# Kernel tuning notes

Measured on AMD Instinct MI355X. Metric: run time of the kernel, lower is better.

## Reference

```python
import jax, jax.numpy as jnp
import numpy as np
import math

NUM_HEADS = 16
FOCUS_FACTOR = 1.35  # 1.0 + congestion_level(0.3) + packet_loss(0.05)


def setup_inputs() -> dict:
    key = jax.random.key(0)
    ks = jax.random.split(key, 6)
    B, S, D = 2, 2048, 1024
    s = 1.0 / math.sqrt(D)
    return {
        "x": jax.random.normal(ks[0], (B, S, D), jnp.float32),
        "mask": jnp.ones((B, 1, S, S), jnp.int32),
        "Wq": jax.random.normal(ks[1], (D, D), jnp.float32) * s,
        "bq": jnp.zeros((D,), jnp.float32),
        "Wk": jax.random.normal(ks[2], (D, D), jnp.float32) * s,
        "bk": jnp.zeros((D,), jnp.float32),
        "Wv": jax.random.normal(ks[3], (D, D), jnp.float32) * s,
        "bv": jnp.zeros((D,), jnp.float32),
        "Wo": jax.random.normal(ks[4], (D, D), jnp.float32) * s,
        "bo": jnp.zeros((D,), jnp.float32),
    }


def reference(x, mask, Wq, bq, Wk, bk, Wv, bv, Wo, bo):
    B, S, D = x.shape
    H = NUM_HEADS
    hd = D // H
    # linear projections (torch Linear: x @ W^T + b), split heads -> [B,H,S,hd]
    q = (x @ Wq.T + bq).reshape(B, S, H, hd).transpose(0, 2, 1, 3)
    k = (x @ Wk.T + bk).reshape(B, S, H, hd).transpose(0, 2, 1, 3)
    v = (x @ Wv.T + bv).reshape(B, S, H, hd).transpose(0, 2, 1, 3)
    # rotary embedding in the source is an identity pass-through
    scores = jnp.einsum("bhqd,bhkd->bhqk", q, k) / math.sqrt(hd)
    scores = jnp.where(mask == 0, jnp.float32(-1e9), scores)
    scores = scores * jnp.float32(FOCUS_FACTOR)  # network focus factor
    attn = jax.nn.softmax(scores, axis=-1)  # dropout is identity in eval
    attended = jnp.einsum("bhqk,bhkd->bhqd", attn, v)
    attended = attended.transpose(0, 2, 1, 3).reshape(B, S, D)
    out = attended @ Wo.T + bo
    avg_attention = attn.mean(axis=1)  # [B, S, S]
    return out, avg_attention
```

## Files before the change

### kernel.cpp

```cpp
#include <hip/hip_runtime.h>
#include <cstdint>

typedef __bf16 bf16x8 __attribute__((ext_vector_type(8)));
typedef __bf16 bf16x4 __attribute__((ext_vector_type(4)));
typedef short  s16x8  __attribute__((ext_vector_type(8)));
typedef float  f32x4  __attribute__((ext_vector_type(4)));
typedef unsigned int uint32;
typedef uint32 u32x2 __attribute__((ext_vector_type(2)));
typedef unsigned long long u64;

#define SB 2048
#define DD 1024
#define HH 16
#define HDD 64
#define BB 2
#define C2LOG 0.2434547882f
#define NEGBIG2 (-1.9476383e9f)

__device__ __forceinline__ ushort f2bf(float f){
  uint32 u = __builtin_bit_cast(uint32, f);
  u += 0x7fffu + ((u >> 16) & 1u);
  return (ushort)(u >> 16);
}
__device__ __forceinline__ bf16x8 ldb128(const void* p){
  return __builtin_bit_cast(bf16x8, *(const s16x8*)p);
}
__device__ __forceinline__ void gl_lds16(const void* g, void* l){
  __builtin_amdgcn_global_load_lds((const __attribute__((address_space(1))) void*)g,
                                   (__attribute__((address_space(3))) void*)l, 16, 0, 0);
}
__device__ __forceinline__ float exp2r(float x){
  float r; asm("v_exp_f32 %0, %1" : "=v"(r) : "v"(x)); return r;
}

__global__ __launch_bounds__(256) void k_prep(
    const float* __restrict__ x, const int* __restrict__ mask,
    const float* __restrict__ Wq, const float* __restrict__ Wk,
    const float* __restrict__ Wv, const float* __restrict__ Wo,
    ushort* __restrict__ xb, u64* __restrict__ bits,
    ushort* __restrict__ wqb, ushort* __restrict__ wkb,
    ushort* __restrict__ wvb, ushort* __restrict__ wob)
{
  int bid = blockIdx.x;
  if (bid < 32768){
    int i = bid * 256 + threadIdx.x;
    u64 bm = __ballot(mask[i] != 0);
    if ((threadIdx.x & 63) == 0) bits[i >> 6] = bm;
  } else if (bid < 36864){
    int i = (bid - 32768) * 256 + threadIdx.x;
    float4 v = ((const float4*)x)[i];
    ushort4 o;
    o.x = f2bf(v.x); o.y = f2bf(v.y); o.z = f2bf(v.z); o.w = f2bf(v.w);
    ((ushort4*)xb)[i] = o;
  } else {
    int sub = bid - 36864;
    int zz = sub >> 10;
    const float* in = (zz == 0) ? Wq : (zz == 1) ? Wk : (zz == 2) ? Wv : Wo;
    ushort* out     = (zz == 0) ? wqb : (zz == 1) ? wkb : (zz == 2) ? wvb : wob;
    int i = (sub & 1023) * 256 + threadIdx.x;
    float4 v = ((const float4*)in)[i];
    ushort4 o;
    o.x = f2bf(v.x); o.y = f2bf(v.y); o.z = f2bf(v.z); o.w = f2bf(v.w);
    ((ushort4*)out)[i] = o;
  }
}

template<int MODE>
__device__ __forceinline__ void gemm_body(
    const ushort* __restrict__ A, const ushort* __restrict__ W,
    const float* __restrict__ bias, float scl,
    ushort* __restrict__ outp, float* __restrict__ outf,
    int rowBase, int colBase, ushort* lsA, ushort* lsB)
{
  const int t = threadIdx.x;
  const int l = t & 63, w = t >> 6;
  const int g16 = l >> 4, r16 = l & 15;
  const int wr = w >> 1, wc = w & 1;
  f32x4 zero = {0.f, 0.f, 0.f, 0.f};
  f32x4 acc[4][4];
  #pragma unroll
  for (int m = 0; m < 4; m++)
    #pragma unroll
    for (int n = 0; n < 4; n++) acc[m][n] = zero;

  auto stage = [&](int kt, int buf){
    #pragma unroll
    for (int i = 0; i < 2; i++){
      int c = t + i * 256;
      int row = c >> 2, cin = c & 3;
      int g = cin ^ ((row >> 1) & 3);
      gl_lds16(A + (size_t)(rowBase + row) * DD + kt * 32 + g * 8, (char*)lsA + buf * 8192 + c * 16);
      gl_lds16(W + (size_t)(colBase + row) * DD + kt * 32 + g * 8, (char*)lsB + buf * 8192 + c * 16);
    }
  };
  stage(0, 0);
  int cur = 0;
  for (int kt = 0; kt < 32; ++kt){
    __syncthreads();
    if (kt + 1 < 32) stage(kt + 1, cur ^ 1);
    bf16x8 af[4], bfr[4];
    #pragma unroll
    for (int m = 0; m < 4; m++){
      int row = wr * 64 + m * 16 + r16;
      af[m] = ldb128((char*)lsA + cur * 8192 + row * 64 + ((g16 ^ ((row >> 1) & 3)) << 4));
    }
    #pragma unroll
    for (int n = 0; n < 4; n++){
      int row = wc * 64 + n * 16 + r16;
      bfr[n] = ldb128((char*)lsB + cur * 8192 + row * 64 + ((g16 ^ ((row >> 1) & 3)) << 4));
    }
    #pragma unroll
    for (int m = 0; m < 4; m++)
      #pragma unroll
      for (int n = 0; n < 4; n++)
        acc[m][n] = __builtin_amdgcn_mfma_f32_16x16x32_bf16(af[m], bfr[n], acc[m][n], 0, 0, 0);
    cur ^= 1;
  }
  #pragma unroll
  for (int m = 0; m < 4; m++){
    #pragma unroll
    for (int n = 0; n < 4; n++){
      int ng = colBase + wc * 64 + n * 16 + r16;
      float bval = bias[ng];
      if (MODE == 2){
        int h = ng >> 6, d = ng & 63;
        int s0 = rowBase + wr * 64 + m * 16 + g16 * 4;
        int b = s0 >> 11, s = s0 & 2047;
        ushort4 o;
        o.x = f2bf((acc[m][n][0] + bval) * scl);
        o.y = f2bf((acc[m][n][1] + bval) * scl);
        o.z = f2bf((acc[m][n][2] + bval) * scl);
        o.w = f2bf((acc[m][n][3] + bval) * scl);
        *(ushort4*)(outp + ((size_t)(b * HH + h) * HDD + d) * SB + s) = o;
      } else {
        #pragma unroll
        for (int j = 0; j < 4; j++){
          int r = rowBase + wr * 64 + m * 16 + g16 * 4 + j;
          float v = (acc[m][n][j] + bval) * scl;
          if (MODE == 0){
            int h = ng >> 6, d = ng & 63;
            int b = r >> 11, s = r & 2047;
            outp[(((size_t)(b * HH + h) * SB + s) << 6) + d] = f2bf(v);
          } else {
            outf[(size_t)r * DD + ng] = v;
          }
        }
      }
    }
  }
}

__device__ __forceinline__ void xcd_patch2(int bid, int& rowBase, int& colBase){
  int xcd = bid & 7, i = bid >> 3;
  rowBase = ((xcd & 3) * 8 + (i & 7)) * 128;
  colBase = ((xcd >> 2) * 4 + (i >> 3)) * 128;
}

__global__ __launch_bounds__(256) void k_gemm_qkv(
    const ushort* __restrict__ A,
    const ushort* __restrict__ Wq, const ushort* __restrict__ Wk, const ushort* __restrict__ Wv,
    const float* __restrict__ bq, const float* __restrict__ bk, const float* __restrict__ bv,
    ushort* __restrict__ Q, ushort* __restrict__ K, ushort* __restrict__ Vt)
{
  __shared__ ushort lsA[2][4096];
  __shared__ ushort lsB[2][4096];
  int rowBase, colBase;
  xcd_patch2(blockIdx.x + blockIdx.y * 8, rowBase, colBase);
  int z = blockIdx.z;
  if (z == 0)      gemm_body<0>(A, Wq, bq, C2LOG, Q, nullptr, rowBase, colBase, &lsA[0][0], &lsB[0][0]);
  else if (z == 1) gemm_body<0>(A, Wk, bk, 1.0f, K, nullptr, rowBase, colBase, &lsA[0][0], &lsB[0][0]);
  else             gemm_body<2>(A, Wv, bv, 1.0f, Vt, nullptr, rowBase, colBase, &lsA[0][0], &lsB[0][0]);
}

__device__ __forceinline__ void stage_kv2(const ushort* __restrict__ Kp,
                                          const ushort* __restrict__ Vp,
                                          ushort* dK, ushort* dV, int t){
  #pragma unroll
  for (int i = 0; i < 2; ++i){
    int c = t + 512 * i;
    int r = c >> 3, g = (c & 7) ^ (r & 7);
    gl_lds16(Kp + (size_t)r * HDD + g * 8, (char*)dK + c * 16);
  }
  #pragma unroll
  for (int i = 0; i < 2; ++i){
    int c = t + 512 * i;
    int r = c >> 4, cc = c & 15;
    int g = ((cc & 7) ^ (r & 7)) | (cc & 8);
    gl_lds16(Vp + (size_t)r * SB + g * 8, (char*)dV + c * 16);
  }
}

__global__ __launch_bounds__(512) void k_flash(
    const ushort* __restrict__ Q, const ushort* __restrict__ K, const ushort* __restrict__ Vt,
    const u64* __restrict__ mbits,
    ushort* __restrict__ att, float* __restrict__ ilarr)
{
  __shared__ ushort lsK[2][8192];
  __shared__ ushort lsV[2][10240];
  __shared__ ushort lsP[8][2048];
  const int t = threadIdx.x;
  const int l = t & 63, w = t >> 6;
  const int g16 = l >> 4, r16 = l & 15;
  const int bid = blockIdx.x;
  const int qt = (bid >> 3) & 7;
  const int hb = (bid >> 6) * 8 + (bid & 7);
  const int h = hb & 15, b = hb >> 4;
  const size_t ho = ((size_t)(b * HH + h)) * SB * HDD;
  const int qa = qt * 256 + w * 32 + r16;
  const int qb = qa + 16;

  bf16x8 aqa[2], aqb[2];
  #pragma unroll
  for (int ks = 0; ks < 2; ++ks){
    aqa[ks] = ldb128(Q + ho + (size_t)qa * HDD + ks * 32 + g16 * 8);
    aqb[ks] = ldb128(Q + ho + (size_t)qb * HDD + ks * 32 + g16 * 8);
  }
  const u64* mpa = mbits + ((size_t)b * SB + qa) * 32;
  const u64* mpb = mbits + ((size_t)b * SB + qb) * 32;

  f32x4 zero = {0.f, 0.f, 0.f, 0.f};
  f32x4 accA[4], accB[4], accLA = zero, accLB = zero;
  #pragma unroll
  for (int c = 0; c < 4; c++){ accA[c] = zero; accB[c] = zero; }

  if (t < 256) lsV[t >> 7][8192 + (t & 127)] = 0x3F80;

  const ushort* Kb = K + ho;
  const ushort* Vb = Vt + ho;
  stage_kv2(Kb, Vb, &lsK[0][0], &lsV[0][0], t);

  int cur = 0;
  for (int kk = 0; kk < 16; ++kk){
    __syncthreads();
    if (kk + 1 < 16)
      stage_kv2(Kb + (size_t)(kk + 1) * 128 * HDD, Vb + (size_t)(kk + 1) * 128,
                &lsK[cur ^ 1][0], &lsV[cur ^ 1][0], t);

    #pragma unroll
    for (int h2 = 0; h2 < 2; ++h2){
      const char* lk = (const char*)&lsK[cur][0] + h2 * 8192;
      const char* lv = (const char*)&lsV[cur][0] + h2 * 128;
      char* lp = (char*)&lsP[w][0];

      f32x4 za[4], zb[4];
      __builtin_amdgcn_s_setprio(1);
      #pragma unroll
      for (int f = 0; f < 4; ++f){
        za[f] = zero; zb[f] = zero;
        int row = 16 * f + r16;
        #pragma unroll
        for (int ks = 0; ks < 2; ++ks){
          bf16x8 kf = ldb128(lk + row * 128 + ((((ks << 2) + g16) ^ (row & 7)) << 4));
          za[f] = __builtin_amdgcn_mfma_f32_16x16x32_bf16(kf, aqa[ks], za[f], 0, 0, 0);
          zb[f] = __builtin_amdgcn_mfma_f32_16x16x32_bf16(kf, aqb[ks], zb[f], 0, 0, 0);
        }
      }
      __builtin_amdgcn_s_setprio(0);

      u64 mwa = mpa[2 * kk + h2], mwb = mpb[2 * kk + h2];
      float pa[4][4], pb[4][4];
      if (__all((mwa & mwb) == ~0ull)){
        #pragma unroll
        for (int f = 0; f < 4; ++f)
          #pragma unroll
          for (int j = 0; j < 4; ++j){
            pa[f][j] = exp2r(za[f][j]);
            pb[f][j] = exp2r(zb[f][j]);
          }
      } else {
        #pragma unroll
        for (int f = 0; f < 4; ++f)
          #pragma unroll
          for (int j = 0; j < 4; ++j){
            int bit = 16 * f + 4 * g16 + j;
            pa[f][j] = exp2r(((mwa >> bit) & 1ull) ? za[f][j] : NEGBIG2);
            pb[f][j] = exp2r(((mwb >> bit) & 1ull) ? zb[f][j] : NEGBIG2);
          }
      }

      {
        int wba = r16 * 128 + ((g16 & 1) << 3);
        int wbb = (r16 + 16) * 128 + ((g16 & 1) << 3);
        #pragma unroll
        for (int f = 0; f < 4; ++f){
          bf16x4 va_ = { (__bf16)pa[f][0], (__bf16)pa[f][1], (__bf16)pa[f][2], (__bf16)pa[f][3] };
          bf16x4 vb_ = { (__bf16)pb[f][0], (__bf16)pb[f][1], (__bf16)pb[f][2], (__bf16)pb[f][3] };
          int sw = ((2 * f + (g16 >> 1)) ^ (r16 & 7)) << 4;
          *(u32x2*)(lp + wba + sw) = __builtin_bit_cast(u32x2, va_);
          *(u32x2*)(lp + wbb + sw) = __builtin_bit_cast(u32x2, vb_);
        }
      }
      bf16x8 pfA[2], pfB[2];
      #pragma unroll
      for (int ks = 0; ks < 2; ++ks){
        int sw = (((ks << 2) + g16) ^ (r16 & 7)) << 4;
        pfA[ks] = ldb128(lp + r16 * 128 + sw);
        pfB[ks] = ldb128(lp + (r16 + 16) * 128 + sw);
      }

      __builtin_amdgcn_s_setprio(1);
      #pragma unroll
      for (int c = 0; c < 4; ++c){
        int row = 16 * c + r16;
        #pragma unroll
        for (int ks = 0; ks < 2; ++ks){
          bf16x8 vf = ldb128(lv + row * 256 + ((((ks << 2) + g16) ^ (row & 7)) << 4));
          accA[c] = __builtin_amdgcn_mfma_f32_16x16x32_bf16(vf, pfA[ks], accA[c], 0, 0, 0);
          accB[c] = __builtin_amdgcn_mfma_f32_16x16x32_bf16(vf, pfB[ks], accB[c], 0, 0, 0);
        }
      }
      {
        int row = 64 + r16;
        #pragma unroll
        for (int ks = 0; ks < 2; ++ks){
          bf16x8 of = ldb128(lv + row * 256 + ((((ks << 2) + g16) ^ (row & 7)) << 4));
          accLA = __builtin_amdgcn_mfma_f32_16x16x32_bf16(of, pfA[ks], accLA, 0, 0, 0);
          accLB = __builtin_amdgcn_mfma_f32_16x16x32_bf16(of, pfB[ks], accLB, 0, 0, 0);
        }
      }
      __builtin_amdgcn_s_setprio(0);
    }
    cur ^= 1;
  }

  float ila = 1.0f / __shfl(accLA[0], r16);
  float ilb = 1.0f / __shfl(accLB[0], r16);
  #pragma unroll
  for (int c = 0; c < 4; ++c){
    ushort4 oa, ob;
    oa.x = f2bf(accA[c][0] * ila); oa.y = f2bf(accA[c][1] * ila);
    oa.z = f2bf(accA[c][2] * ila); oa.w = f2bf(accA[c][3] * ila);
    ob.x = f2bf(accB[c][0] * ilb); ob.y = f2bf(accB[c][1] * ilb);
    ob.z = f2bf(accB[c][2] * ilb); ob.w = f2bf(accB[c][3] * ilb);
    *(ushort4*)(att + ((size_t)b * SB + qa) * DD + h * HDD + c * 16 + 4 * g16) = oa;
    *(ushort4*)(att + ((size_t)b * SB + qb) * DD + h * HDD + c * 16 + 4 * g16) = ob;
  }
  if (g16 == 0){
    ilarr[(size_t)(b * HH + h) * SB + qa] = ila;
    ilarr[(size_t)(b * HH + h) * SB + qb] = ilb;
  }
}

__global__ __launch_bounds__(512) void k_avg_out(
    const ushort* __restrict__ att, const ushort* __restrict__ wob,
    const float* __restrict__ bo, float* __restrict__ out,
    const ushort* __restrict__ Q, const ushort* __restrict__ K,
    const u64* __restrict__ mbits,
    const float* __restrict__ ilarr, float* __restrict__ avg)
{
  __shared__ ushort smem[32768];
  const int bid = blockIdx.x;
  const int t = threadIdx.x;

  if (bid < 256){
    int rowBase, colBase;
    xcd_patch2(bid, rowBase, colBase);
    if (t < 256){
      gemm_body<1>(att, wob, bo, 1.0f, nullptr, out, rowBase, colBase,
                   smem, smem + 8192);
    } else {
      #pragma unroll 1
      for (int k = 0; k < 32; ++k) __syncthreads();
    }
    return;
  }

  const int bid2 = bid - 256;
  const int kt = bid2 & 15, qt = (bid2 >> 4) & 15, b = bid2 >> 8;
  ushort* lsQ0 = smem;
  ushort* lsK0 = smem + 16384;
  const int l = t & 63, w = t >> 6;
  const int g16 = l >> 4, r16 = l & 15;
  const int qbase = qt * 128, kbase = kt * 128;
  const int qr0 = qbase + w * 16 + g16 * 4;

  u64 mw[4][2];
  #pragma unroll
  for (int j = 0; j < 4; j++){
    mw[j][0] = mbits[((size_t)b * SB + qr0 + j) * 32 + 2 * kt];
    mw[j][1] = mbits[((size_t)b * SB + qr0 + j) * 32 + 2 * kt + 1];
  }
  bool fast = __all((mw[0][0] & mw[0][1] & mw[1][0] & mw[1][1] &
                     mw[2][0] & mw[2][1] & mw[3][0] & mw[3][1]) == ~0ull);

  f32x4 zero = {0.f, 0.f, 0.f, 0.f};
  f32x4 acc[8];
  #pragma unroll
  for (int f = 0; f < 8; f++) acc[f] = zero;

  const size_t hstep = (size_t)SB * HDD;
  const ushort* Qp = Q + (size_t)b * HH * hstep + (size_t)qbase * HDD;
  const ushort* Kp = K + (size_t)b * HH * hstep + (size_t)kbase * HDD;

  for (int hh = 0; hh < 8; ++hh){
    __syncthreads();
    #pragma unroll
    for (int p = 0; p < 2; ++p){
      int h = 2 * hh + p;
      #pragma unroll
      for (int i = 0; i < 2; ++i){
        int c = t + i * 512;
        int r = c >> 3, g = (c & 7) ^ (r & 7);
        gl_lds16(Qp + (size_t)h * hstep + (size_t)r * HDD + g * 8, (char*)(lsQ0 + p * 8192) + c * 16);
        gl_lds16(Kp + (size_t)h * hstep + (size_t)r * HDD + g * 8, (char*)(lsK0 + p * 8192) + c * 16);
      }
    }
    __syncthreads();

    #pragma unroll
    for (int p = 0; p < 2; ++p){
      int h = 2 * hh + p;
      int qrow = w * 16 + r16;
      bf16x8 a0 = ldb128((char*)(lsQ0 + p * 8192) + qrow * 128 + (((0 + g16) ^ (qrow & 7)) << 4));
      bf16x8 a1 = ldb128((char*)(lsQ0 + p * 8192) + qrow * 128 + (((4 + g16) ^ (qrow & 7)) << 4));
      float ilh[4];
      #pragma unroll
      for (int j = 0; j < 4; j++)
        ilh[j] = ilarr[(size_t)(b * HH + h) * SB + qr0 + j];

      #pragma unroll
      for (int f = 0; f < 8; ++f){
        int row = 16 * f + r16;
        bf16x8 b0 = ldb128((char*)(lsK0 + p * 8192) + row * 128 + (((0 + g16) ^ (row & 7)) << 4));
        bf16x8 b1 = ldb128((char*)(lsK0 + p * 8192) + row * 128 + (((4 + g16) ^ (row & 7)) << 4));
        f32x4 z = zero;
        z = __builtin_amdgcn_mfma_f32_16x16x32_bf16(a0, b0, z, 0, 0, 0);
        z = __builtin_amdgcn_mfma_f32_16x16x32_bf16(a1, b1, z, 0, 0, 0);
        if (fast){
          #pragma unroll
          for (int j = 0; j < 4; j++)
            acc[f][j] += exp2r(z[j]) * ilh[j];
        } else {
          int kl = 16 * f + r16;
          int word = kl >> 6, bit = kl & 63;
          #pragma unroll
          for (int j = 0; j < 4; j++){
            float s = ((mw[j][word] >> bit) & 1ull) ? z[j] : NEGBIG2;
            acc[f][j] += exp2r(s) * ilh[j];
          }
        }
      }
    }
  }
  #pragma unroll
  for (int f = 0; f < 8; f++)
    #pragma unroll
    for (int j = 0; j < 4; j++){
      int qr = qr0 + j;
      int kc = kbase + 16 * f + r16;
      avg[((size_t)b * SB + qr) * SB + kc] = acc[f][j] * 0.0625f;
    }
}

extern "C" void kernel_launch(void* const* d_in, const int* in_sizes, int n_in,
                              void* d_out, int out_size, void* d_ws, size_t ws_size,
                              hipStream_t stream)
{
  const float* x  = (const float*)d_in[0];
  const int* mask = (const int*)d_in[1];
  const float* Wq = (const float*)d_in[2];
  const float* bq = (const float*)d_in[3];
  const float* Wk = (const float*)d_in[4];
  const float* bk = (const float*)d_in[5];
  const float* Wv = (const float*)d_in[6];
  const float* bv = (const float*)d_in[7];
  const float* Wo = (const float*)d_in[8];
  const float* bo = (const float*)d_in[9];
  float* out = (float*)d_out;
  float* avg = out + (size_t)BB * SB * DD;

  char* ws = (char*)d_ws;
  ushort* xb   = (ushort*)(ws);
  ushort* wqb  = (ushort*)(ws + (8ull  << 20));
  ushort* wkb  = (ushort*)(ws + (10ull << 20));
  ushort* wvb  = (ushort*)(ws + (12ull << 20));
  ushort* wob  = (ushort*)(ws + (14ull << 20));
  ushort* Qb   = (ushort*)(ws + (16ull << 20));
  ushort* Kb   = (ushort*)(ws + (24ull << 20));
  ushort* Vtb  = (ushort*)(ws + (32ull << 20));
  ushort* att  = (ushort*)(ws + (40ull << 20));
  float*  ilarr= (float*) (ws + (48ull << 20));
  u64*    mbits= (u64*)   (ws + (49ull << 20));

  k_prep<<<40960, 256, 0, stream>>>(x, mask, Wq, Wk, Wv, Wo,
                                    xb, mbits, wqb, wkb, wvb, wob);
  k_gemm_qkv<<<dim3(8, 32, 3), 256, 0, stream>>>(xb, wqb, wkb, wvb,
                                                 bq, bk, bv, Qb, Kb, Vtb);
  k_flash<<<256, 512, 0, stream>>>(Qb, Kb, Vtb, mbits, att, ilarr);
  k_avg_out<<<768, 512, 0, stream>>>(att, wob, bo, out, Qb, Kb, mbits, ilarr, avg);
}
```

Before: 160.4 us.

## Enlarge avg-attention and output-projection tiles in fused kernel, halving block count

The output projection section now uses 128 blocks with 512 threads, each computing a 128x256 tile with an inline double-buffered MFMA loop. Before, it used 256 blocks whose upper half of threads did nothing. The avg-attention section now covers 256 query rows per block, so each staged K tile is reused for two query groups, and it loads one head per iteration instead of two. This cuts redundant K loads and idle threads, but leaves 384 blocks, which may underfill the GPU. It also raises register pressure and moves the masked-path mbits reads inside the inner loop.

```diff
diff --git a/kernel.cpp b/kernel.cpp
--- a/kernel.cpp
+++ b/kernel.cpp
@@ -348,96 +348,163 @@
     const u64* __restrict__ mbits,
     const float* __restrict__ ilarr, float* __restrict__ avg)
 {
-  __shared__ ushort smem[32768];
+  __shared__ ushort smem[24576];
   const int bid = blockIdx.x;
   const int t = threadIdx.x;
-
-  if (bid < 256){
-    int rowBase, colBase;
-    xcd_patch2(bid, rowBase, colBase);
-    if (t < 256){
-      gemm_body<1>(att, wob, bo, 1.0f, nullptr, out, rowBase, colBase,
-                   smem, smem + 8192);
-    } else {
-      #pragma unroll 1
-      for (int k = 0; k < 32; ++k) __syncthreads();
-    }
-    return;
-  }
-
-  const int bid2 = bid - 256;
-  const int kt = bid2 & 15, qt = (bid2 >> 4) & 15, b = bid2 >> 8;
-  ushort* lsQ0 = smem;
-  ushort* lsK0 = smem + 16384;
   const int l = t & 63, w = t >> 6;
   const int g16 = l >> 4, r16 = l & 15;
-  const int qbase = qt * 128, kbase = kt * 128;
+  f32x4 zero = {0.f, 0.f, 0.f, 0.f};
+
+  if (bid < 128){
+    int xcd = bid & 7, i = bid >> 3;
+    int rowBase = ((xcd & 3) * 8 + (i & 7)) * 128;
+    int colBase = ((xcd >> 2) * 2 + (i >> 3)) * 256;
+    ushort* lsA = smem;
+    ushort* lsB = smem + 8192;
+    const int wr = w >> 2, wc = w & 3;
+    f32x4 acc[4][4];
+    #pragma unroll
+    for (int m = 0; m < 4; m++)
+      #pragma unroll
+      for (int n = 0; n < 4; n++) acc[m][n] = zero;
+
+    auto stage = [&](int kt, int buf){
+      {
+        int c = t;
+        int row = c >> 2, cin = c & 3;
+        int g = cin ^ ((row >> 1) & 3);
+        gl_lds16(att + (size_t)(rowBase + row) * DD + kt * 32 + g * 8,
+                 (char*)lsA + buf * 8192 + c * 16);
+      }
+      #pragma unroll
+      for (int ii = 0; ii < 2; ++ii){
+        int c = t + ii * 512;
+        int row = c >> 2, cin = c & 3;
+        int g = cin ^ ((row >> 1) & 3);
+        gl_lds16(wob + (size_t)(colBase + row) * DD + kt * 32 + g * 8,
+                 (char*)lsB + buf * 16384 + c * 16);
+      }
+    };
+    stage(0, 0);
+    int cur = 0;
+    for (int kt = 0; kt < 32; ++kt){
+      __syncthreads();
+      if (kt + 1 < 32) stage(kt + 1, cur ^ 1);
+      bf16x8 af[4], bfr[4];
+      #pragma unroll
+      for (int m = 0; m < 4; m++){
+        int row = wr * 64 + m * 16 + r16;
+        af[m] = ldb128((char*)lsA + cur * 8192 + row * 64 + ((g16 ^ ((row >> 1) & 3)) << 4));
+      }
+      #pragma unroll
+      for (int n = 0; n < 4; n++){
+        int row = wc * 64 + n * 16 + r16;
+        bfr[n] = ldb128((char*)lsB + cur * 16384 + row * 64 + ((g16 ^ ((row >> 1) & 3)) << 4));
+      }
+      #pragma unroll
+      for (int m = 0; m < 4; m++)
+        #pragma unroll
+        for (int n = 0; n < 4; n++)
+          acc[m][n] = __builtin_amdgcn_mfma_f32_16x16x32_bf16(af[m], bfr[n], acc[m][n], 0, 0, 0);
+      cur ^= 1;
+    }
+    #pragma unroll
+    for (int m = 0; m < 4; m++)
+      #pragma unroll
+      for (int n = 0; n < 4; n++){
+        int ng = colBase + wc * 64 + n * 16 + r16;
+        float bval = bo[ng];
+        #pragma unroll
+        for (int j = 0; j < 4; j++){
+          int r = rowBase + wr * 64 + m * 16 + g16 * 4 + j;
+          out[(size_t)r * DD + ng] = acc[m][n][j] + bval;
+        }
+      }
+    return;
+  }
+
+  const int bid2 = bid - 128;
+  const int kt = bid2 & 15, qt = (bid2 >> 4) & 7, b = bid2 >> 7;
+  ushort* lsQ = smem;
+  ushort* lsK = smem + 16384;
+  const int qbase = qt * 256, kbase = kt * 128;
   const int qr0 = qbase + w * 16 + g16 * 4;
-
-  u64 mw[4][2];
-  #pragma unroll
-  for (int j = 0; j < 4; j++){
-    mw[j][0] = mbits[((size_t)b * SB + qr0 + j) * 32 + 2 * kt];
-    mw[j][1] = mbits[((size_t)b * SB + qr0 + j) * 32 + 2 * kt + 1];
-  }
-  bool fast = __all((mw[0][0] & mw[0][1] & mw[1][0] & mw[1][1] &
-                     mw[2][0] & mw[2][1] & mw[3][0] & mw[3][1]) == ~0ull);
-
-  f32x4 zero = {0.f, 0.f, 0.f, 0.f};
-  f32x4 acc[8];
-  #pragma unroll
-  for (int f = 0; f < 8; f++) acc[f] = zero;
+  const int qr1 = qr0 + 128;
+
+  u64 andv = ~0ull;
+  #pragma unroll
+  for (int j = 0; j < 4; ++j)
+    #pragma unroll
+    for (int wd = 0; wd < 2; ++wd){
+      andv &= mbits[((size_t)b * SB + qr0 + j) * 32 + 2 * kt + wd];
+      andv &= mbits[((size_t)b * SB + qr1 + j) * 32 + 2 * kt + wd];
+    }
+  bool fast = __all(andv == ~0ull);
+
+  f32x4 accA[8], accB[8];
+  #pragma unroll
+  for (int f = 0; f < 8; f++){ accA[f] = zero; accB[f] = zero; }
 
   const size_t hstep = (size_t)SB * HDD;
   const ushort* Qp = Q + (size_t)b * HH * hstep + (size_t)qbase * HDD;
   const ushort* Kp = K + (size_t)b * HH * hstep + (size_t)kbase * HDD;
 
-  for (int hh = 0; hh < 8; ++hh){
+  for (int h = 0; h < HH; ++h){
     __syncthreads();
     #pragma unroll
-    for (int p = 0; p < 2; ++p){
-      int h = 2 * hh + p;
-      #pragma unroll
-      for (int i = 0; i < 2; ++i){
-        int c = t + i * 512;
-        int r = c >> 3, g = (c & 7) ^ (r & 7);
-        gl_lds16(Qp + (size_t)h * hstep + (size_t)r * HDD + g * 8, (char*)(lsQ0 + p * 8192) + c * 16);
-        gl_lds16(Kp + (size_t)h * hstep + (size_t)r * HDD + g * 8, (char*)(lsK0 + p * 8192) + c * 16);
-      }
+    for (int i = 0; i < 4; ++i){
+      int c = t + i * 512;
+      int r = c >> 3, g = (c & 7) ^ (r & 7);
+      gl_lds16(Qp + (size_t)h * hstep + (size_t)r * HDD + g * 8, (char*)lsQ + c * 16);
+    }
+    #pragma unroll
+    for (int i = 0; i < 2; ++i){
+      int c = t + i * 512;
+      int r = c >> 3, g = (c & 7) ^ (r & 7);
+      gl_lds16(Kp + (size_t)h * hstep + (size_t)r * HDD + g * 8, (char*)lsK + c * 16);
     }
     __syncthreads();
 
-    #pragma unroll
-    for (int p = 0; p < 2; ++p){
-      int h = 2 * hh + p;
-      int qrow = w * 16 + r16;
-      bf16x8 a0 = ldb128((char*)(lsQ0 + p * 8192) + qrow * 128 + (((0 + g16) ^ (qrow & 7)) << 4));
-      bf16x8 a1 = ldb128((char*)(lsQ0 + p * 8192) + qrow * 128 + (((4 + g16) ^ (qrow & 7)) << 4));
-      float ilh[4];
-      #pragma unroll
-      for (int j = 0; j < 4; j++)
-        ilh[j] = ilarr[(size_t)(b * HH + h) * SB + qr0 + j];
-
-      #pragma unroll
-      for (int f = 0; f < 8; ++f){
-        int row = 16 * f + r16;
-        bf16x8 b0 = ldb128((char*)(lsK0 + p * 8192) + row * 128 + (((0 + g16) ^ (row & 7)) << 4));
-        bf16x8 b1 = ldb128((char*)(lsK0 + p * 8192) + row * 128 + (((4 + g16) ^ (row & 7)) << 4));
-        f32x4 z = zero;
-        z = __builtin_amdgcn_mfma_f32_16x16x32_bf16(a0, b0, z, 0, 0, 0);
-        z = __builtin_amdgcn_mfma_f32_16x16x32_bf16(a1, b1, z, 0, 0, 0);
-        if (fast){
-          #pragma unroll
-          for (int j = 0; j < 4; j++)
-            acc[f][j] += exp2r(z[j]) * ilh[j];
-        } else {
-          int kl = 16 * f + r16;
-          int word = kl >> 6, bit = kl & 63;
-          #pragma unroll
-          for (int j = 0; j < 4; j++){
-            float s = ((mw[j][word] >> bit) & 1ull) ? z[j] : NEGBIG2;
-            acc[f][j] += exp2r(s) * ilh[j];
-          }
+    int qrow = w * 16 + r16;
+    int qrow2 = qrow + 128;
+    bf16x8 a0 = ldb128((char*)lsQ + qrow * 128 + (((0 + g16) ^ (qrow & 7)) << 4));
+    bf16x8 a1 = ldb128((char*)lsQ + qrow * 128 + (((4 + g16) ^ (qrow & 7)) << 4));
+    bf16x8 c0 = ldb128((char*)lsQ + qrow2 * 128 + (((0 + g16) ^ (qrow2 & 7)) << 4));
+    bf16x8 c1 = ldb128((char*)lsQ + qrow2 * 128 + (((4 + g16) ^ (qrow2 & 7)) << 4));
+    float ilhA[4], ilhB[4];
+    #pragma unroll
+    for (int j = 0; j < 4; j++){
+      ilhA[j] = ilarr[(size_t)(b * HH + h) * SB + qr0 + j];
+      ilhB[j] = ilarr[(size_t)(b * HH + h) * SB + qr1 + j];
+    }
+
+    #pragma unroll
+    for (int f = 0; f < 8; ++f){
+      int row = 16 * f + r16;
+      bf16x8 b0 = ldb128((char*)lsK + row * 128 + (((0 + g16) ^ (row & 7)) << 4));
+      bf16x8 b1 = ldb128((char*)lsK + row * 128 + (((4 + g16) ^ (row & 7)) << 4));
+      f32x4 zA = zero, zB = zero;
+      zA = __builtin_amdgcn_mfma_f32_16x16x32_bf16(a0, b0, zA, 0, 0, 0);
+      zA = __builtin_amdgcn_mfma_f32_16x16x32_bf16(a1, b1, zA, 0, 0, 0);
+      zB = __builtin_amdgcn_mfma_f32_16x16x32_bf16(c0, b0, zB, 0, 0, 0);
+      zB = __builtin_amdgcn_mfma_f32_16x16x32_bf16(c1, b1, zB, 0, 0, 0);
+      if (fast){
+        #pragma unroll
+        for (int j = 0; j < 4; j++){
+          accA[f][j] += exp2r(zA[j]) * ilhA[j];
+          accB[f][j] += exp2r(zB[j]) * ilhB[j];
+        }
+      } else {
+        int kl = 16 * f + r16;
+        int word = kl >> 6, bit = kl & 63;
+        #pragma unroll
+        for (int j = 0; j < 4; j++){
+          u64 mA = mbits[((size_t)b * SB + qr0 + j) * 32 + 2 * kt + word];
+          u64 mB = mbits[((size_t)b * SB + qr1 + j) * 32 + 2 * kt + word];
+          float sA = ((mA >> bit) & 1ull) ? zA[j] : NEGBIG2;
+          float sB = ((mB >> bit) & 1ull) ? zB[j] : NEGBIG2;
+          accA[f][j] += exp2r(sA) * ilhA[j];
+          accB[f][j] += exp2r(sB) * ilhB[j];
         }
       }
     }
@@ -446,9 +513,9 @@
   for (int f = 0; f < 8; f++)
     #pragma unroll
     for (int j = 0; j < 4; j++){
-      int qr = qr0 + j;
       int kc = kbase + 16 * f + r16;
-      avg[((size_t)b * SB + qr) * SB + kc] = acc[f][j] * 0.0625f;
+      avg[((size_t)b * SB + qr0 + j) * SB + kc] = accA[f][j] * 0.0625f;
+      avg[((size_t)b * SB + qr1 + j) * SB + kc] = accB[f][j] * 0.0625f;
     }
 }
 
@@ -487,5 +554,5 @@
   k_gemm_qkv<<<dim3(8, 32, 3), 256, 0, stream>>>(xb, wqb, wkb, wvb,
                                                  bq, bk, bv, Qb, Kb, Vtb);
   k_flash<<<256, 512, 0, stream>>>(Qb, Kb, Vtb, mbits, att, ilarr);
-  k_avg_out<<<768, 512, 0, stream>>>(att, wob, bo, out, Qb, Kb, mbits, ilarr, avg);
-}
+  k_avg_out<<<384, 512, 0, stream>>>(att, wob, bo, out, Qb, Kb, mbits, ilarr, avg);
+}
```

Result: slower. 182.2 us (+13.6%).
